# Performance work log

Hardware: AMD Instinct MI355X
Metric: run time of the kernel (lower is better)

## Reference

```python
import jax, jax.numpy as jnp
import numpy as np

B, F_DIM, P, C, H = 16, 256, 8192, 96, 256


def setup_inputs() -> dict:
    key = jax.random.key(0)
    ks = jax.random.split(key, 8)
    seg_feat = jax.random.normal(ks[0], (B, F_DIM, P), dtype=jnp.float32)
    seg_label = jax.random.randint(ks[1], (B, P), 0, C, dtype=jnp.int64 if jax.config.read('jax_enable_x64') else jnp.int32)
    s1 = 1.0 / np.sqrt(F_DIM)
    s2 = 1.0 / np.sqrt(H)
    w1 = jax.random.uniform(ks[2], (F_DIM, H), jnp.float32, -s1, s1)
    b1 = jax.random.uniform(ks[3], (H,), jnp.float32, -s1, s1)
    w2 = jax.random.uniform(ks[4], (H, H), jnp.float32, -s2, s2)
    b2 = jax.random.uniform(ks[5], (H,), jnp.float32, -s2, s2)
    w_logit = jax.random.uniform(ks[6], (H, C), jnp.float32, -s2, s2)
    b_logit = jax.random.uniform(ks[7], (C,), jnp.float32, -s2, s2)
    return dict(seg_feat=seg_feat, seg_label=seg_label, w1=w1, b1=b1,
                w2=w2, b2=b2, w_logit=w_logit, b_logit=b_logit)


def _pool_by_class(seg_feat, seg_label, num_classes):
    # seg_feat: [B, F, P], seg_label: [B, P] -> pooled [B*C, F]
    b, f, p = seg_feat.shape
    seg_ids = (jnp.arange(b, dtype=seg_label.dtype)[:, None] * num_classes
               + seg_label).reshape(-1)                       # [B*P]
    feat = seg_feat.transpose(0, 2, 1).reshape(b * p, f)      # [B*P, F]
    segmax = jax.ops.segment_max(feat, seg_ids, num_segments=b * num_classes)
    counts = jax.ops.segment_sum(jnp.ones((b * p,), feat.dtype), seg_ids,
                                 num_segments=b * num_classes)  # [B*C]
    counts = counts[:, None]
    # torch: max over points of feat * onehot -> zeros from other classes
    # participate in the max unless the class covers ALL points; empty
    # classes pool to 0 (max of all zeros).
    pooled = jnp.where(counts == 0, 0.0,
                       jnp.where(counts == p, segmax, jnp.maximum(segmax, 0.0)))
    return pooled


def reference(seg_feat, seg_label, w1, b1, w2, b2, w_logit, b_logit):
    num_classes = w_logit.shape[1]
    pooled = _pool_by_class(seg_feat, seg_label, num_classes)   # [B*C, F]
    # feat_mlp: Linear+ReLU x2 (dropout_prob=0), then part_logit
    h = jax.nn.relu(pooled @ w1 + b1)
    h = jax.nn.relu(h @ w2 + b2)
    part_pred = h @ w_logit + b_logit                           # [B*C, C]
    b = seg_feat.shape[0]
    part_batch = jnp.repeat(jnp.arange(b), num_classes)
    part_label = jnp.tile(jnp.arange(num_classes), b)
    return part_pred, part_label, part_batch
```

## Files before the change

### kernel.cpp

```cpp
#include <hip/hip_runtime.h>

#define B 16
#define F_DIM 256
#define P 8192
#define C 96
#define H 256
#define NSEG (B * C)

__device__ __forceinline__ unsigned f2key(float x) {
    unsigned u = __float_as_uint(x);
    return (u & 0x80000000u) ? ~u : (u | 0x80000000u);
}
__device__ __forceinline__ float key2f(unsigned k) {
    unsigned u = (k & 0x80000000u) ? (k & 0x7FFFFFFFu) : ~k;
    return __uint_as_float(u);
}

__global__ __launch_bounds__(256) void count_kernel(const int* __restrict__ label,
                                                    int* __restrict__ counts) {
    __shared__ int hist[C];
    const int b = blockIdx.x;
    const int t = threadIdx.x;
    if (t < C) hist[t] = 0;
    __syncthreads();
    const int* lrow = label + b * P;
    for (int p = t; p < P; p += 256) {
        atomicAdd(&hist[lrow[p]], 1);
    }
    __syncthreads();
    if (t < C) counts[b * C + t] = hist[t];
}

__global__ __launch_bounds__(256) void pool_kernel(const float* __restrict__ feat,
                                                   const int* __restrict__ label,
                                                   const int* __restrict__ counts,
                                                   float* __restrict__ pooled) {
    __shared__ unsigned smax[C];
    const int blk = blockIdx.x;
    const int b = blk >> 8;
    const int f = blk & 255;
    const int t = threadIdx.x;
    if (t < C) smax[t] = 0u;
    __syncthreads();

    const float4* frow4 = (const float4*)(feat + ((size_t)b * F_DIM + f) * P);
    const int4*   lrow4 = (const int4*)(label + (size_t)b * P);

    float4 v[8];
    int4   c[8];
    #pragma unroll
    for (int j = 0; j < 8; ++j) v[j] = frow4[t + j * 256];
    #pragma unroll
    for (int j = 0; j < 8; ++j) c[j] = lrow4[t + j * 256];

    #pragma unroll
    for (int j = 0; j < 8; ++j) {
        atomicMax(&smax[c[j].x], f2key(v[j].x));
        atomicMax(&smax[c[j].y], f2key(v[j].y));
        atomicMax(&smax[c[j].z], f2key(v[j].z));
        atomicMax(&smax[c[j].w], f2key(v[j].w));
    }
    __syncthreads();

    if (t < C) {
        const int cnt = counts[b * C + t];
        const float v = key2f(smax[t]);
        float r = (cnt == 0) ? 0.0f : ((cnt == P) ? v : fmaxf(v, 0.0f));
        pooled[(size_t)(b * C + t) * F_DIM + f] = r;
    }
}

template <int COLS, int RELU, int OUTW>
__global__ __launch_bounds__(256, 3) void dense_kernel(const float* __restrict__ x,
                                                       const float* __restrict__ w,
                                                       const float* __restrict__ bias,
                                                       float* __restrict__ y,
                                                       float* __restrict__ tails) {
    constexpr int NQ = COLS / 4;
    __shared__ float xs[8][H];
    __shared__ float ps[8][COLS][17];
    const int t = threadIdx.x;
    const int row0 = blockIdx.x * 8;
    const int bj0 = blockIdx.y * COLS;

    {
        int i0 = t, i1 = t + 256;
        ((float4*)xs)[i0] = ((const float4*)(x + (size_t)row0 * H))[i0];
        ((float4*)xs)[i1] = ((const float4*)(x + (size_t)row0 * H))[i1];
    }
    __syncthreads();

    const int s = t >> 4;
    const int jq = t & 15;

    if (jq < NQ) {
        const float4* w4 = (const float4*)w;
        constexpr int WS4 = OUTW / 4;
        const int wq = (bj0 >> 2) + jq;
        const int kbase = s * 16;
        float4 acc[8];
        #pragma unroll
        for (int r = 0; r < 8; ++r) acc[r] = (float4){0.f, 0.f, 0.f, 0.f};

        #pragma unroll
        for (int i = 0; i < 16; ++i) {
            const int k = kbase + i;
            const float4 wv = w4[k * WS4 + wq];
            #pragma unroll
            for (int r = 0; r < 8; ++r) {
                const float xv = xs[r][k];
                acc[r].x = fmaf(xv, wv.x, acc[r].x);
                acc[r].y = fmaf(xv, wv.y, acc[r].y);
                acc[r].z = fmaf(xv, wv.z, acc[r].z);
                acc[r].w = fmaf(xv, wv.w, acc[r].w);
            }
        }
        #pragma unroll
        for (int r = 0; r < 8; ++r) {
            ps[r][jq * 4 + 0][s] = acc[r].x;
            ps[r][jq * 4 + 1][s] = acc[r].y;
            ps[r][jq * 4 + 2][s] = acc[r].z;
            ps[r][jq * 4 + 3][s] = acc[r].w;
        }
    }
    __syncthreads();

    for (int e = t; e < 8 * COLS; e += 256) {
        const int r = e / COLS, j = e % COLS;
        float v = bias[bj0 + j];
        #pragma unroll
        for (int q = 0; q < 16; ++q) v += ps[r][j][q];
        if (RELU) v = fmaxf(v, 0.0f);
        y[(size_t)(row0 + r) * OUTW + bj0 + j] = v;
    }

    if (tails != nullptr && t < 8) {
        const int row = row0 + t;
        tails[row] = (float)(row % C);
        tails[NSEG + row] = (float)(row / C);
    }
}

extern "C" void kernel_launch(void* const* d_in, const int* in_sizes, int n_in,
                              void* d_out, int out_size, void* d_ws, size_t ws_size,
                              hipStream_t stream) {
    const float* feat  = (const float*)d_in[0];
    const int*   label = (const int*)d_in[1];
    const float* w1    = (const float*)d_in[2];
    const float* b1    = (const float*)d_in[3];
    const float* w2    = (const float*)d_in[4];
    const float* b2    = (const float*)d_in[5];
    const float* wl    = (const float*)d_in[6];
    const float* bl    = (const float*)d_in[7];
    float* out = (float*)d_out;

    char* ws = (char*)d_ws;
    int*   counts = (int*)ws;
    float* pooled = (float*)(ws + 8192);
    float* h1     = (float*)(ws + 8192 + NSEG * H * 4);
    float* h2     = (float*)(ws + 8192 + 2 * NSEG * H * 4);

    count_kernel<<<B, 256, 0, stream>>>(label, counts);
    pool_kernel<<<B * F_DIM, 256, 0, stream>>>(feat, label, counts, pooled);
    dense_kernel<64, 1, H><<<dim3(NSEG / 8, 4), 256, 0, stream>>>(pooled, w1, b1, h1, nullptr);
    dense_kernel<64, 1, H><<<dim3(NSEG / 8, 4), 256, 0, stream>>>(h1, w2, b2, h2, nullptr);
    dense_kernel<48, 0, C><<<dim3(NSEG / 8, 2), 256, 0, stream>>>(h2, wl, bl, out, out + (size_t)NSEG * C);
}
```

Measured before the change: 53.36 us.

## Fuse class counting into pooling and process 8 features per block

Each pooling block now handles 8 feature rows of one batch, loads the labels once and reuses them, and computes the per-class histogram in-block, so the separate count kernel and its launch go away. Feature loads are double-buffered across the 8 rows, and the pooled output is written as float4 pairs. The grid shrinks from 4096 to 512 blocks, which lowers parallelism and memory-level concurrency on a large GPU, and each block runs 8 times as many shared atomics serially.

```diff
diff --git a/kernel.cpp b/kernel.cpp
--- a/kernel.cpp
+++ b/kernel.cpp
@@ -6,6 +6,8 @@
 #define C 96
 #define H 256
 #define NSEG (B * C)
+#define G 8
+#define NFBLK (F_DIM / G)
 
 __device__ __forceinline__ unsigned f2key(float x) {
     unsigned u = __float_as_uint(x);
@@ -16,57 +18,76 @@
     return __uint_as_float(u);
 }
 
-__global__ __launch_bounds__(256) void count_kernel(const int* __restrict__ label,
-                                                    int* __restrict__ counts) {
+__global__ __launch_bounds__(256) void pool_kernel(const float* __restrict__ feat,
+                                                   const int* __restrict__ label,
+                                                   float* __restrict__ pooled) {
+    __shared__ unsigned smax[G][C];
     __shared__ int hist[C];
-    const int b = blockIdx.x;
+    const int blk = blockIdx.x;
+    const int b = blk >> 5;
+    const int f0 = (blk & 31) << 3;
     const int t = threadIdx.x;
+
+    for (int i = t; i < G * C; i += 256) ((unsigned*)smax)[i] = 0u;
     if (t < C) hist[t] = 0;
     __syncthreads();
-    const int* lrow = label + b * P;
-    for (int p = t; p < P; p += 256) {
-        atomicAdd(&hist[lrow[p]], 1);
-    }
-    __syncthreads();
-    if (t < C) counts[b * C + t] = hist[t];
-}
 
-__global__ __launch_bounds__(256) void pool_kernel(const float* __restrict__ feat,
-                                                   const int* __restrict__ label,
-                                                   const int* __restrict__ counts,
-                                                   float* __restrict__ pooled) {
-    __shared__ unsigned smax[C];
-    const int blk = blockIdx.x;
-    const int b = blk >> 8;
-    const int f = blk & 255;
-    const int t = threadIdx.x;
-    if (t < C) smax[t] = 0u;
-    __syncthreads();
-
-    const float4* frow4 = (const float4*)(feat + ((size_t)b * F_DIM + f) * P);
-    const int4*   lrow4 = (const int4*)(label + (size_t)b * P);
-
-    float4 v[8];
-    int4   c[8];
+    const int4* lrow4 = (const int4*)(label + (size_t)b * P);
+    int4 lab[8];
     #pragma unroll
-    for (int j = 0; j < 8; ++j) v[j] = frow4[t + j * 256];
-    #pragma unroll
-    for (int j = 0; j < 8; ++j) c[j] = lrow4[t + j * 256];
+    for (int j = 0; j < 8; ++j) lab[j] = lrow4[t + j * 256];
 
     #pragma unroll
     for (int j = 0; j < 8; ++j) {
-        atomicMax(&smax[c[j].x], f2key(v[j].x));
-        atomicMax(&smax[c[j].y], f2key(v[j].y));
-        atomicMax(&smax[c[j].z], f2key(v[j].z));
-        atomicMax(&smax[c[j].w], f2key(v[j].w));
+        atomicAdd(&hist[lab[j].x], 1);
+        atomicAdd(&hist[lab[j].y], 1);
+        atomicAdd(&hist[lab[j].z], 1);
+        atomicAdd(&hist[lab[j].w], 1);
+    }
+
+    const float4* fbase4 = (const float4*)(feat + ((size_t)b * F_DIM + f0) * P);
+
+    float4 cur[8], nxt[8];
+    #pragma unroll
+    for (int j = 0; j < 8; ++j) cur[j] = fbase4[t + j * 256];
+
+    #pragma unroll 1
+    for (int f = 0; f < G; ++f) {
+        if (f + 1 < G) {
+            #pragma unroll
+            for (int j = 0; j < 8; ++j)
+                nxt[j] = fbase4[(size_t)(f + 1) * (P / 4) + t + j * 256];
+        }
+        #pragma unroll
+        for (int j = 0; j < 8; ++j) {
+            atomicMax(&smax[f][lab[j].x], f2key(cur[j].x));
+            atomicMax(&smax[f][lab[j].y], f2key(cur[j].y));
+            atomicMax(&smax[f][lab[j].z], f2key(cur[j].z));
+            atomicMax(&smax[f][lab[j].w], f2key(cur[j].w));
+        }
+        #pragma unroll
+        for (int j = 0; j < 8; ++j) cur[j] = nxt[j];
     }
     __syncthreads();
 
     if (t < C) {
-        const int cnt = counts[b * C + t];
-        const float v = key2f(smax[t]);
-        float r = (cnt == 0) ? 0.0f : ((cnt == P) ? v : fmaxf(v, 0.0f));
-        pooled[(size_t)(b * C + t) * F_DIM + f] = r;
+        const int cnt = hist[t];
+        float4 lo, hi;
+        float* lv = (float*)&lo;
+        float* hv = (float*)&hi;
+        #pragma unroll
+        for (int f = 0; f < 4; ++f) {
+            const float v = key2f(smax[f][t]);
+            lv[f] = (cnt == 0) ? 0.0f : ((cnt == P) ? v : fmaxf(v, 0.0f));
+        }
+        #pragma unroll
+        for (int f = 4; f < 8; ++f) {
+            const float v = key2f(smax[f][t]);
+            hv[f - 4] = (cnt == 0) ? 0.0f : ((cnt == P) ? v : fmaxf(v, 0.0f));
+        }
+        float* dst = &pooled[(size_t)(b * C + t) * F_DIM + f0];
+        *(float4*)dst = lo;
+        *(float4*)(dst + 4) = hi;
     }
 }
 
@@ -155,13 +176,11 @@
     float* out = (float*)d_out;
 
     char* ws = (char*)d_ws;
-    int*   counts = (int*)ws;
-    float* pooled = (float*)(ws + 8192);
-    float* h1     = (float*)(ws + 8192 + NSEG * H * 4);
-    float* h2     = (float*)(ws + 8192 + 2 * NSEG * H * 4);
+    float* pooled = (float*)ws;
+    float* h1     = (float*)(ws + NSEG * H * 4);
+    float* h2     = (float*)(ws + 2 * NSEG * H * 4);
 
-    count_kernel<<<B, 256, 0, stream>>>(label, counts);
-    pool_kernel<<<B * F_DIM, 256, 0, stream>>>(feat, label, counts, pooled);
+    pool_kernel<<<B * NFBLK, 256, 0, stream>>>(feat, label, pooled);
     dense_kernel<64, 1, H><<<dim3(NSEG / 8, 4), 256, 0, stream>>>(pooled, w1, b1, h1, nullptr);
     dense_kernel<64, 1, H><<<dim3(NSEG / 8, 4), 256, 0, stream>>>(h1, w2, b2, h2, nullptr);
     dense_kernel<48, 0, C><<<dim3(NSEG / 8, 2), 256, 0, stream>>>(h2, wl, bl, out, out + (size_t)NSEG * C);
```

New measurement: 44.32 us, median of 2. 1.2x faster.
